# Kernel tuning notes

Measured on AMD Instinct MI355X. Metric: run time of the kernel, lower is better.

## Reference

```python
import jax, jax.numpy as jnp
import numpy as np

N = 100000   # num nodes
E = 20000    # num hyperedges
D = 128      # feature dim
NNZ = 600000 # incidences
EPS = 1e-5


def setup_inputs() -> dict:
    key = jax.random.key(0)
    ks = jax.random.split(key, 16)
    src = jax.random.randint(ks[0], (NNZ,), 0, N)   # node indices
    edg = jax.random.randint(ks[1], (NNZ,), 0, E)   # hyperedge indices
    edge_index = jnp.stack([src, edg]).astype(jnp.int64)
    node_attr = jax.random.normal(ks[2], (N, D), jnp.float32)
    edge_attr = jax.random.normal(ks[3], (E, D), jnp.float32)  # unused by forward
    inp = {"edge_index": edge_index, "node_attr": node_attr, "edge_attr": edge_attr}
    for l in range(3):
        inp[f"W{l+1}"] = jax.random.normal(ks[4 + l], (D, D), jnp.float32) / np.float32(np.sqrt(D))
        inp[f"b{l+1}"] = jnp.zeros((D,), jnp.float32)
        inp[f"g{l+1}"] = jnp.ones((D,), jnp.float32)
        inp[f"beta{l+1}"] = jnp.zeros((D,), jnp.float32)
    return inp


def _hconv(x, W, b, src, edg):
    # PyG HypergraphConv (no attention): out = D^{-1} H W_e B^{-1} H^T (X Theta) + b, W_e = I
    x = x @ W
    ones = jnp.ones(src.shape, x.dtype)
    deg_n = jax.ops.segment_sum(ones, src, num_segments=N)  # node degree
    deg_e = jax.ops.segment_sum(ones, edg, num_segments=E)  # hyperedge size
    Dinv = jnp.where(deg_n > 0, 1.0 / deg_n, 0.0)
    Binv = jnp.where(deg_e > 0, 1.0 / deg_e, 0.0)
    # node -> hyperedge: m_e = B^{-1} sum_{i in e} x_i
    e_feat = Binv[:, None] * jax.ops.segment_sum(x[src], edg, num_segments=E)
    # hyperedge -> node: out_i = D^{-1} sum_{e ni i} m_e
    out = Dinv[:, None] * jax.ops.segment_sum(e_feat[edg], src, num_segments=N)
    return out + b


def _bn(x, g, beta):
    # BatchNorm1d, training mode (biased variance over nodes)
    mu = jnp.mean(x, axis=0)
    var = jnp.mean((x - mu) ** 2, axis=0)
    return g * (x - mu) / jnp.sqrt(var + EPS) + beta


def reference(edge_index, node_attr, edge_attr,
              W1, b1, g1, beta1, W2, b2, g2, beta2, W3, b3, g3, beta3):
    src, edg = edge_index[0], edge_index[1]
    x = _bn(jax.nn.relu(_hconv(node_attr, W1, b1, src, edg)), g1, beta1)
    x = _bn(jax.nn.relu(_hconv(x, W2, b2, src, edg)), g2, beta2)
    x = _bn(jax.nn.relu(_hconv(x, W3, b3, src, edg)), g3, beta3)
    return x
```

## Files before the change

### kernel.cpp

```cpp
#include <hip/hip_runtime.h>
#include <stdint.h>

#define DIM 128

static inline int cdiv(long a, long b) { return (int)((a + b - 1) / b); }

typedef float f32x4 __attribute__((ext_vector_type(4)));

__device__ __forceinline__ unsigned pk_bf16(float a, float b) {
  unsigned ua = __float_as_uint(a), ub = __float_as_uint(b);
  ua = (ua + 0x7FFFu + ((ua >> 16) & 1u)) >> 16;
  ub = (ub + 0x7FFFu + ((ub >> 16) & 1u)) >> 16;
  return ua | (ub << 16);
}
__device__ __forceinline__ float bf_lo(unsigned u) { return __uint_as_float(u << 16); }
__device__ __forceinline__ float bf_hi(unsigned u) { return __uint_as_float(u & 0xFFFF0000u); }

__global__ __launch_bounds__(256) void count_kernel(
    const int* __restrict__ raw, int* __restrict__ src, int* __restrict__ edg,
    int* __restrict__ cnt, int E, int nnz) {
  bool is64;
  {
    int l = threadIdx.x & 63;
    int v = raw[2 * l + 1];
    unsigned long long m = __ballot(v == 0);
    is64 = (m == ~0ull);
  }
  int g = blockIdx.x * 256 + threadIdx.x;
  if (g < nnz) {
    int s = is64 ? raw[2 * g] : raw[g];
    int e = is64 ? raw[2 * (nnz + g)] : raw[nnz + g];
    src[g] = s;
    edg[g] = e;
    atomicAdd(&cnt[e], 1);
    atomicAdd(&cnt[E + s], 1);
  }
}

__global__ __launch_bounds__(256) void scanA_kernel(
    const int* __restrict__ cnt, int* __restrict__ P, int* __restrict__ BS, int M) {
  __shared__ int lds[256];
  int t = threadIdx.x;
  long base = blockIdx.x * 1024L;
  int v[4], ts = 0;
#pragma unroll
  for (int j = 0; j < 4; ++j) {
    long i = base + t * 4 + j;
    v[j] = (i < M) ? cnt[i] : 0;
    ts += v[j];
  }
  lds[t] = ts;
  __syncthreads();
  for (int off = 1; off < 256; off <<= 1) {
    int x = (t >= off) ? lds[t - off] : 0;
    __syncthreads();
    lds[t] += x;
    __syncthreads();
  }
  int run = lds[t] - ts;
#pragma unroll
  for (int j = 0; j < 4; ++j) {
    long i = base + t * 4 + j;
    if (i < M) P[i] = run;
    run += v[j];
  }
  if (t == 255) BS[blockIdx.x] = lds[255];
}

__global__ void scanB_kernel(int* __restrict__ BS, int* __restrict__ P,
                             int nblocks, int M) {
  if (threadIdx.x == 0) {
    int run = 0;
    for (int i = 0; i < nblocks; ++i) { int x = BS[i]; BS[i] = run; run += x; }
    P[M] = run;
  }
}

__global__ __launch_bounds__(256) void scanC_kernel(
    int* __restrict__ P, const int* __restrict__ BS, int M) {
  long i = blockIdx.x * 256L + threadIdx.x;
  if (i < M) P[i] += BS[i >> 10];
}

__global__ __launch_bounds__(256) void fill_adj_kernel(
    const int* __restrict__ src, const int* __restrict__ edg,
    const int* __restrict__ P, int* __restrict__ cnt,
    int* __restrict__ adj_e, int* __restrict__ adj_n, int E, int nnz) {
  int g = blockIdx.x * 256 + threadIdx.x;
  if (g < nnz) {
    int e = edg[g], s = src[g];
    int pe = P[e] + atomicAdd(&cnt[e], 1);
    adj_e[pe] = s;
    int pn = P[E + s] - nnz + atomicAdd(&cnt[E + s], 1);
    adj_n[pn] = e;
  }
}

__global__ void prep_w_kernel(const float* __restrict__ W,
                              const float* __restrict__ sums,
                              const float* __restrict__ sumsq,
                              const float* __restrict__ gprev,
                              const float* __restrict__ betaprev,
                              float* __restrict__ Wp, float* __restrict__ rvec,
                              int has_aff, float inv_n) {
  __shared__ float sa[DIM], sd[DIM];
  int j = threadIdx.x;
  if (has_aff) {
    float mu = sums[j] * inv_n;
    float var = fmaf(sumsq[j], inv_n, -mu * mu);
    float a = gprev[j] * rsqrtf(var + 1e-5f);
    sa[j] = a;
    sd[j] = fmaf(-mu, a, betaprev[j]);
  } else {
    sa[j] = 1.0f;
    sd[j] = 0.0f;
  }
  __syncthreads();
  float racc = 0.0f;
  for (int c = 0; c < DIM; ++c) {
    float w = W[c * DIM + j];
    Wp[c * DIM + j] = sa[c] * w;
    racc = fmaf(sd[c], w, racc);
  }
  rvec[j] = racc;
}

__global__ __launch_bounds__(256) void edge_gather_f32_kernel(
    const float4* __restrict__ X4, const int* __restrict__ P,
    const int* __restrict__ adj_e, float* __restrict__ ag, int E) {
  int slot = threadIdx.x >> 5;
  int l = threadIdx.x & 31;
  int e = blockIdx.x * 8 + slot;
  if (e >= E) return;
  int p0 = P[e], p1 = P[e + 1];
  float4 a = {0.f, 0.f, 0.f, 0.f};
  int kl = p1 - 1;
  for (int k = p0; k < p1; k += 8) {
    int n0 = adj_e[min(k, kl)];
    int n1 = adj_e[min(k + 1, kl)];
    int n2 = adj_e[min(k + 2, kl)];
    int n3 = adj_e[min(k + 3, kl)];
    int n4 = adj_e[min(k + 4, kl)];
    int n5 = adj_e[min(k + 5, kl)];
    int n6 = adj_e[min(k + 6, kl)];
    int n7 = adj_e[min(k + 7, kl)];
    float4 q0 = X4[(size_t)n0 * 32 + l];
    float4 q1 = X4[(size_t)n1 * 32 + l];
    float4 q2 = X4[(size_t)n2 * 32 + l];
    float4 q3 = X4[(size_t)n3 * 32 + l];
    float4 q4 = X4[(size_t)n4 * 32 + l];
    float4 q5 = X4[(size_t)n5 * 32 + l];
    float4 q6 = X4[(size_t)n6 * 32 + l];
    float4 q7 = X4[(size_t)n7 * 32 + l];
    a.x += ((q0.x + q1.x) + (q2.x + q3.x)) + ((q4.x + q5.x) + (q6.x + q7.x));
    a.y += ((q0.y + q1.y) + (q2.y + q3.y)) + ((q4.y + q5.y) + (q6.y + q7.y));
    a.z += ((q0.z + q1.z) + (q2.z + q3.z)) + ((q4.z + q5.z) + (q6.z + q7.z));
    a.w += ((q0.w + q1.w) + (q2.w + q3.w)) + ((q4.w + q5.w) + (q6.w + q7.w));
  }
  int deg = p1 - p0;
  if (deg > 0) {
    int extra = ((deg + 7) & ~7) - deg;
    if (extra) {
      float4 ql = X4[(size_t)adj_e[kl] * 32 + l];
      float ex = (float)extra;
      a.x -= ex * ql.x; a.y -= ex * ql.y; a.z -= ex * ql.z; a.w -= ex * ql.w;
    }
  }
  float binv = (deg > 0) ? 1.0f / (float)deg : 0.0f;
  f32x4 o;
  o.x = a.x * binv; o.y = a.y * binv; o.z = a.z * binv; o.w = a.w * binv;
  __builtin_nontemporal_store(o, &((f32x4*)ag)[(size_t)e * 32 + l]);
}

__global__ __launch_bounds__(256) void edge_gather_bf16_kernel(
    const uint2* __restrict__ xh, const int* __restrict__ P,
    const int* __restrict__ adj_e, float* __restrict__ ag, int E) {
  int slot = threadIdx.x >> 5;
  int l = threadIdx.x & 31;
  int e = blockIdx.x * 8 + slot;
  if (e >= E) return;
  int p0 = P[e], p1 = P[e + 1];
  float4 a = {0.f, 0.f, 0.f, 0.f};
  int kl = p1 - 1;
  for (int k = p0; k < p1; k += 8) {
    int n0 = adj_e[min(k, kl)];
    int n1 = adj_e[min(k + 1, kl)];
    int n2 = adj_e[min(k + 2, kl)];
    int n3 = adj_e[min(k + 3, kl)];
    int n4 = adj_e[min(k + 4, kl)];
    int n5 = adj_e[min(k + 5, kl)];
    int n6 = adj_e[min(k + 6, kl)];
    int n7 = adj_e[min(k + 7, kl)];
    uint2 q0 = xh[(size_t)n0 * 32 + l];
    uint2 q1 = xh[(size_t)n1 * 32 + l];
    uint2 q2 = xh[(size_t)n2 * 32 + l];
    uint2 q3 = xh[(size_t)n3 * 32 + l];
    uint2 q4 = xh[(size_t)n4 * 32 + l];
    uint2 q5 = xh[(size_t)n5 * 32 + l];
    uint2 q6 = xh[(size_t)n6 * 32 + l];
    uint2 q7 = xh[(size_t)n7 * 32 + l];
    a.x += ((bf_lo(q0.x) + bf_lo(q1.x)) + (bf_lo(q2.x) + bf_lo(q3.x))) +
           ((bf_lo(q4.x) + bf_lo(q5.x)) + (bf_lo(q6.x) + bf_lo(q7.x)));
    a.y += ((bf_hi(q0.x) + bf_hi(q1.x)) + (bf_hi(q2.x) + bf_hi(q3.x))) +
           ((bf_hi(q4.x) + bf_hi(q5.x)) + (bf_hi(q6.x) + bf_hi(q7.x)));
    a.z += ((bf_lo(q0.y) + bf_lo(q1.y)) + (bf_lo(q2.y) + bf_lo(q3.y))) +
           ((bf_lo(q4.y) + bf_lo(q5.y)) + (bf_lo(q6.y) + bf_lo(q7.y)));
    a.w += ((bf_hi(q0.y) + bf_hi(q1.y)) + (bf_hi(q2.y) + bf_hi(q3.y))) +
           ((bf_hi(q4.y) + bf_hi(q5.y)) + (bf_hi(q6.y) + bf_hi(q7.y)));
  }
  int deg = p1 - p0;
  if (deg > 0) {
    int extra = ((deg + 7) & ~7) - deg;
    if (extra) {
      uint2 ql = xh[(size_t)adj_e[kl] * 32 + l];
      float ex = (float)extra;
      a.x -= ex * bf_lo(ql.x); a.y -= ex * bf_hi(ql.x);
      a.z -= ex * bf_lo(ql.y); a.w -= ex * bf_hi(ql.y);
    }
  }
  float binv = (deg > 0) ? 1.0f / (float)deg : 0.0f;
  f32x4 o;
  o.x = a.x * binv; o.y = a.y * binv; o.z = a.z * binv; o.w = a.w * binv;
  __builtin_nontemporal_store(o, &((f32x4*)ag)[(size_t)e * 32 + l]);
}

__global__ __launch_bounds__(256) void gemm128_kernel(
    const float* __restrict__ X, const float* __restrict__ Wp,
    const float* __restrict__ rvec, const int* __restrict__ Pdeg,
    unsigned* __restrict__ Yh, int nrows) {
  __shared__ float sW[32 * DIM];
  __shared__ float sX[DIM * 36];
  const int t = threadIdx.x;
  const int row0 = blockIdx.x * DIM;
  const int tx = t & 15, ty = t >> 4;
  const int col0 = tx * 8, lr0 = ty * 8;
  float acc[8][8];
#pragma unroll
  for (int i = 0; i < 8; ++i)
#pragma unroll
    for (int j = 0; j < 8; ++j) acc[i][j] = 0.0f;

  for (int kc = 0; kc < 4; ++kc) {
    __syncthreads();
    {
      const float4* W4 = (const float4*)(Wp + kc * 32 * DIM);
      float4* sW4 = (float4*)sW;
#pragma unroll
      for (int i = 0; i < 4; ++i) sW4[t + i * 256] = W4[t + i * 256];
    }
#pragma unroll
    for (int i = 0; i < 4; ++i) {
      int q = t + i * 256;
      int rr = q >> 3, kq = q & 7;
      int gr = row0 + rr; if (gr >= nrows) gr = nrows - 1;
      float4 v = *(const float4*)&X[(size_t)gr * DIM + kc * 32 + kq * 4];
      *(float4*)&sX[rr * 36 + kq * 4] = v;
    }
    __syncthreads();
    for (int kk = 0; kk < 32; ++kk) {
      float4 w0 = *(const float4*)&sW[kk * DIM + col0];
      float4 w1 = *(const float4*)&sW[kk * DIM + col0 + 4];
      float wv[8] = {w0.x, w0.y, w0.z, w0.w, w1.x, w1.y, w1.z, w1.w};
      float xv[8];
#pragma unroll
      for (int i = 0; i < 8; ++i) xv[i] = sX[(lr0 + i) * 36 + kk];
#pragma unroll
      for (int i = 0; i < 8; ++i)
#pragma unroll
        for (int j = 0; j < 8; ++j) acc[i][j] = fmaf(xv[i], wv[j], acc[i][j]);
    }
  }
  float4 r0 = *(const float4*)&rvec[col0];
  float4 r1 = *(const float4*)&rvec[col0 + 4];
#pragma unroll
  for (int i = 0; i < 8; ++i) {
    int gr = row0 + lr0 + i;
    if (gr < nrows) {
      float nz = (Pdeg[gr + 1] > Pdeg[gr]) ? 1.0f : 0.0f;
      float o0x = (acc[i][0] + r0.x) * nz, o0y = (acc[i][1] + r0.y) * nz;
      float o0z = (acc[i][2] + r0.z) * nz, o0w = (acc[i][3] + r0.w) * nz;
      float o1x = (acc[i][4] + r1.x) * nz, o1y = (acc[i][5] + r1.y) * nz;
      float o1z = (acc[i][6] + r1.z) * nz, o1w = (acc[i][7] + r1.w) * nz;
      uint4 st;
      st.x = pk_bf16(o0x, o0y);
      st.y = pk_bf16(o0z, o0w);
      st.z = pk_bf16(o1x, o1y);
      st.w = pk_bf16(o1z, o1w);
      *(uint4*)&Yh[(size_t)gr * 64 + (col0 >> 1)] = st;
    }
  }
}

__global__ __launch_bounds__(256) void node_gather_kernel(
    const uint2* __restrict__ ef, const int* __restrict__ P,
    const int* __restrict__ adj_n, const float* __restrict__ b,
    uint2* __restrict__ zh, float* __restrict__ sum,
    float* __restrict__ sumsq, int E, int N, int nnz) {
  __shared__ float lsum[DIM], lsumsq[DIM];
  int t = threadIdx.x;
  if (t < DIM) { lsum[t] = 0.f; lsumsq[t] = 0.f; }
  __syncthreads();
  int slot = t >> 5;
  int l = t & 31;
  float4 bc = ((const float4*)b)[l];
  float4 s1 = {0.f, 0.f, 0.f, 0.f}, s2 = {0.f, 0.f, 0.f, 0.f};
  for (int i = blockIdx.x * 8 + slot; i < N; i += gridDim.x * 8) {
    int p0 = P[E + i] - nnz, p1 = P[E + i + 1] - nnz;
    float4 a = {0.f, 0.f, 0.f, 0.f};
    int kl = p1 - 1;
    for (int k = p0; k < p1; k += 8) {
      int e0 = adj_n[min(k, kl)];
      int e1 = adj_n[min(k + 1, kl)];
      int e2 = adj_n[min(k + 2, kl)];
      int e3 = adj_n[min(k + 3, kl)];
      int e4 = adj_n[min(k + 4, kl)];
      int e5 = adj_n[min(k + 5, kl)];
      int e6 = adj_n[min(k + 6, kl)];
      int e7 = adj_n[min(k + 7, kl)];
      uint2 q0 = ef[(size_t)e0 * 32 + l];
      uint2 q1 = ef[(size_t)e1 * 32 + l];
      uint2 q2 = ef[(size_t)e2 * 32 + l];
      uint2 q3 = ef[(size_t)e3 * 32 + l];
      uint2 q4 = ef[(size_t)e4 * 32 + l];
      uint2 q5 = ef[(size_t)e5 * 32 + l];
      uint2 q6 = ef[(size_t)e6 * 32 + l];
      uint2 q7 = ef[(size_t)e7 * 32 + l];
      a.x += ((bf_lo(q0.x) + bf_lo(q1.x)) + (bf_lo(q2.x) + bf_lo(q3.x))) +
             ((bf_lo(q4.x) + bf_lo(q5.x)) + (bf_lo(q6.x) + bf_lo(q7.x)));
      a.y += ((bf_hi(q0.x) + bf_hi(q1.x)) + (bf_hi(q2.x) + bf_hi(q3.x))) +
             ((bf_hi(q4.x) + bf_hi(q5.x)) + (bf_hi(q6.x) + bf_hi(q7.x)));
      a.z += ((bf_lo(q0.y) + bf_lo(q1.y)) + (bf_lo(q2.y) + bf_lo(q3.y))) +
             ((bf_lo(q4.y) + bf_lo(q5.y)) + (bf_lo(q6.y) + bf_lo(q7.y)));
      a.w += ((bf_hi(q0.y) + bf_hi(q1.y)) + (bf_hi(q2.y) + bf_hi(q3.y))) +
             ((bf_hi(q4.y) + bf_hi(q5.y)) + (bf_hi(q6.y) + bf_hi(q7.y)));
    }
    int deg = p1 - p0;
    if (deg > 0) {
      int extra = ((deg + 7) & ~7) - deg;
      if (extra) {
        uint2 ql = ef[(size_t)adj_n[kl] * 32 + l];
        float ex = (float)extra;
        a.x -= ex * bf_lo(ql.x); a.y -= ex * bf_hi(ql.x);
        a.z -= ex * bf_lo(ql.y); a.w -= ex * bf_hi(ql.y);
      }
    }
    float dinv = (deg > 0) ? 1.0f / (float)deg : 0.0f;
    float4 v;
    v.x = fmaxf(fmaf(dinv, a.x, bc.x), 0.f);
    v.y = fmaxf(fmaf(dinv, a.y, bc.y), 0.f);
    v.z = fmaxf(fmaf(dinv, a.z, bc.z), 0.f);
    v.w = fmaxf(fmaf(dinv, a.w, bc.w), 0.f);
    uint2 o;
    o.x = pk_bf16(v.x, v.y);
    o.y = pk_bf16(v.z, v.w);
    zh[(size_t)i * 32 + l] = o;
    s1.x += v.x; s1.y += v.y; s1.z += v.z; s1.w += v.w;
    s2.x = fmaf(v.x, v.x, s2.x); s2.y = fmaf(v.y, v.y, s2.y);
    s2.z = fmaf(v.z, v.z, s2.z); s2.w = fmaf(v.w, v.w, s2.w);
  }
  int c0 = l * 4;
  atomicAdd(&lsum[c0 + 0], s1.x); atomicAdd(&lsum[c0 + 1], s1.y);
  atomicAdd(&lsum[c0 + 2], s1.z); atomicAdd(&lsum[c0 + 3], s1.w);
  atomicAdd(&lsumsq[c0 + 0], s2.x); atomicAdd(&lsumsq[c0 + 1], s2.y);
  atomicAdd(&lsumsq[c0 + 2], s2.z); atomicAdd(&lsumsq[c0 + 3], s2.w);
  __syncthreads();
  if (t < DIM) {
    atomicAdd(&sum[t], lsum[t]);
    atomicAdd(&sumsq[t], lsumsq[t]);
  }
}

__global__ void finalize_bn_kernel(const float* __restrict__ sum,
                                   const float* __restrict__ sumsq,
                                   const float* __restrict__ g,
                                   const float* __restrict__ beta,
                                   float* __restrict__ aff_a, float* __restrict__ aff_d,
                                   int n) {
  int c = threadIdx.x;
  float inv_n = 1.0f / (float)n;
  float mu = sum[c] * inv_n;
  float var = fmaf(sumsq[c], inv_n, -mu * mu);
  float a = g[c] * rsqrtf(var + 1e-5f);
  aff_a[c] = a;
  aff_d[c] = fmaf(-mu, a, beta[c]);
}

__global__ __launch_bounds__(256) void apply_affine_kernel(
    const uint2* __restrict__ zh, const float* __restrict__ aff_a,
    const float* __restrict__ aff_d, float* __restrict__ out, long total4) {
  long i = blockIdx.x * 256L + threadIdx.x;
  if (i >= total4) return;
  int c4 = (int)(i & 31);
  float4 a = ((const float4*)aff_a)[c4];
  float4 d = ((const float4*)aff_d)[c4];
  uint2 q = zh[i];
  f32x4 o;
  o.x = fmaf(a.x, bf_lo(q.x), d.x);
  o.y = fmaf(a.y, bf_hi(q.x), d.y);
  o.z = fmaf(a.z, bf_lo(q.y), d.z);
  o.w = fmaf(a.w, bf_hi(q.y), d.w);
  __builtin_nontemporal_store(o, &((f32x4*)out)[i]);
}

extern "C" void kernel_launch(void* const* d_in, const int* in_sizes, int n_in,
                              void* d_out, int out_size, void* d_ws, size_t ws_size,
                              hipStream_t stream) {
  const int NNZv = in_sizes[0] / 2;
  const int Nv   = in_sizes[1] / DIM;
  const int Ev   = in_sizes[2] / DIM;
  const int* eidx_raw = (const int*)d_in[0];
  const float* node_attr = (const float*)d_in[1];

  float* bufE  = (float*)d_ws;
  float* Wp    = bufE + (size_t)Ev * DIM;
  float* rvec  = Wp + DIM * DIM;
  float* sums  = rvec + 128;
  float* sumsq = sums + 128;
  float* aff_a = sumsq + 128;
  float* aff_d = aff_a + 128;
  int* src   = (int*)(aff_d + 128);
  int* edg   = src + NNZv;
  int* cnt   = edg + NNZv;
  int* P     = cnt + (((size_t)Ev + Nv + 3) & ~(size_t)3);
  int* BS    = P + (((size_t)Ev + Nv + 1 + 3) & ~(size_t)3);
  int* adj_e = BS + 256;
  int* adj_n = adj_e + NNZv;
  unsigned* efh = (unsigned*)src;
  uint2* xh = (uint2*)(adj_n + NNZv);

  const int M = Ev + Nv;
  const int nbA = cdiv(M, 1024);
  const float inv_n = 1.0f / (float)Nv;

  hipMemsetAsync(cnt, 0, (size_t)M * 4, stream);
  count_kernel<<<cdiv(NNZv, 256), 256, 0, stream>>>(eidx_raw, src, edg, cnt, Ev, NNZv);
  scanA_kernel<<<nbA, 256, 0, stream>>>(cnt, P, BS, M);
  scanB_kernel<<<1, 64, 0, stream>>>(BS, P, nbA, M);
  scanC_kernel<<<cdiv(M, 256), 256, 0, stream>>>(P, BS, M);
  hipMemsetAsync(cnt, 0, (size_t)M * 4, stream);
  fill_adj_kernel<<<cdiv(NNZv, 256), 256, 0, stream>>>(src, edg, P, cnt, adj_e, adj_n, Ev, NNZv);

  for (int l = 0; l < 3; ++l) {
    const float* W     = (const float*)d_in[3 + l * 4];
    const float* b     = (const float*)d_in[4 + l * 4];
    const float* gprev    = (const float*)d_in[5 + (l > 0 ? l - 1 : 0) * 4];
    const float* betaprev = (const float*)d_in[6 + (l > 0 ? l - 1 : 0) * 4];

    prep_w_kernel<<<1, 128, 0, stream>>>(W, sums, sumsq, gprev, betaprev,
                                         Wp, rvec, l > 0 ? 1 : 0, inv_n);
    if (l == 0)
      edge_gather_f32_kernel<<<cdiv(Ev, 8), 256, 0, stream>>>(
          (const float4*)node_attr, P, adj_e, bufE, Ev);
    else
      edge_gather_bf16_kernel<<<cdiv(Ev, 8), 256, 0, stream>>>(
          xh, P, adj_e, bufE, Ev);
    gemm128_kernel<<<cdiv(Ev, DIM), 256, 0, stream>>>(bufE, Wp, rvec, P, efh, Ev);
    hipMemsetAsync(sums, 0, 256 * 4, stream);
    node_gather_kernel<<<2048, 256, 0, stream>>>(
        (const uint2*)efh, P, adj_n, b, xh, sums, sumsq, Ev, Nv, NNZv);
  }
  {
    const float* g2    = (const float*)d_in[5 + 2 * 4];
    const float* beta2 = (const float*)d_in[6 + 2 * 4];
    finalize_bn_kernel<<<1, 128, 0, stream>>>(sums, sumsq, g2, beta2, aff_a, aff_d, Nv);
  }
  apply_affine_kernel<<<cdiv((long)Nv * 32, 256), 256, 0, stream>>>(
      xh, aff_a, aff_d, (float*)d_out, (long)Nv * 32);
}
```

Before: 714.4 us.

## Use zero sentinel rows for gather padding and fold small launches into neighbours

```diff
diff --git a/kernel.cpp b/kernel.cpp
--- a/kernel.cpp
+++ b/kernel.cpp
@@ -15,6 +15,17 @@
 }
 __device__ __forceinline__ float bf_lo(unsigned u) { return __uint_as_float(u << 16); }
 __device__ __forceinline__ float bf_hi(unsigned u) { return __uint_as_float(u & 0xFFFF0000u); }
+
+__device__ __forceinline__ void acc8(float4& a, const uint2* q) {
+  a.x += ((bf_lo(q[0].x) + bf_lo(q[1].x)) + (bf_lo(q[2].x) + bf_lo(q[3].x))) +
+         ((bf_lo(q[4].x) + bf_lo(q[5].x)) + (bf_lo(q[6].x) + bf_lo(q[7].x)));
+  a.y += ((bf_hi(q[0].x) + bf_hi(q[1].x)) + (bf_hi(q[2].x) + bf_hi(q[3].x))) +
+         ((bf_hi(q[4].x) + bf_hi(q[5].x)) + (bf_hi(q[6].x) + bf_hi(q[7].x)));
+  a.z += ((bf_lo(q[0].y) + bf_lo(q[1].y)) + (bf_lo(q[2].y) + bf_lo(q[3].y))) +
+         ((bf_lo(q[4].y) + bf_lo(q[5].y)) + (bf_lo(q[6].y) + bf_lo(q[7].y)));
+  a.w += ((bf_hi(q[0].y) + bf_hi(q[1].y)) + (bf_hi(q[2].y) + bf_hi(q[3].y))) +
+         ((bf_hi(q[4].y) + bf_hi(q[5].y)) + (bf_hi(q[6].y) + bf_hi(q[7].y)));
+}
 
 __global__ __launch_bounds__(256) void count_kernel(
     const int* __restrict__ raw, int* __restrict__ src, int* __restrict__ edg,
@@ -77,9 +88,12 @@
 }
 
 __global__ __launch_bounds__(256) void scanC_kernel(
-    int* __restrict__ P, const int* __restrict__ BS, int M) {
+    int* __restrict__ P, const int* __restrict__ BS, int* __restrict__ cnt, int M) {
   long i = blockIdx.x * 256L + threadIdx.x;
-  if (i < M) P[i] += BS[i >> 10];
+  if (i < M) {
+    P[i] += BS[i >> 10];
+    cnt[i] = 0;
+  }
 }
 
 __global__ __launch_bounds__(256) void fill_adj_kernel(
@@ -96,33 +110,41 @@
   }
 }
 
-__global__ void prep_w_kernel(const float* __restrict__ W,
-                              const float* __restrict__ sums,
-                              const float* __restrict__ sumsq,
-                              const float* __restrict__ gprev,
-                              const float* __restrict__ betaprev,
-                              float* __restrict__ Wp, float* __restrict__ rvec,
-                              int has_aff, float inv_n) {
+__global__ __launch_bounds__(1024) void prep_w_kernel(
+    const float* __restrict__ W, float* __restrict__ sums,
+    float* __restrict__ sumsq, const float* __restrict__ gprev,
+    const float* __restrict__ betaprev, float* __restrict__ Wp,
+    float* __restrict__ rvec, int has_aff, float inv_n) {
   __shared__ float sa[DIM], sd[DIM];
-  int j = threadIdx.x;
-  if (has_aff) {
-    float mu = sums[j] * inv_n;
-    float var = fmaf(sumsq[j], inv_n, -mu * mu);
-    float a = gprev[j] * rsqrtf(var + 1e-5f);
-    sa[j] = a;
-    sd[j] = fmaf(-mu, a, betaprev[j]);
-  } else {
-    sa[j] = 1.0f;
-    sd[j] = 0.0f;
-  }
-  __syncthreads();
-  float racc = 0.0f;
-  for (int c = 0; c < DIM; ++c) {
+  __shared__ float red[1024];
+  int t = threadIdx.x;
+  if (t < DIM) {
+    float a = 1.0f, d = 0.0f;
+    if (has_aff) {
+      float mu = sums[t] * inv_n;
+      float var = fmaf(sumsq[t], inv_n, -mu * mu);
+      a = gprev[t] * rsqrtf(var + 1e-5f);
+      d = fmaf(-mu, a, betaprev[t]);
+    }
+    sa[t] = a; sd[t] = d;
+  }
+  __syncthreads();
+  if (t < DIM) { sums[t] = 0.f; sumsq[t] = 0.f; }
+  int j = t & 127, grp = t >> 7;
+  float racc = 0.f;
+  for (int c = grp; c < DIM; c += 8) {
     float w = W[c * DIM + j];
     Wp[c * DIM + j] = sa[c] * w;
     racc = fmaf(sd[c], w, racc);
   }
-  rvec[j] = racc;
+  red[t] = racc;
+  __syncthreads();
+  if (t < DIM) {
+    float r = 0.f;
+#pragma unroll
+    for (int g2 = 0; g2 < 8; ++g2) r += red[j + g2 * 128];
+    rvec[j] = r;
+  }
 }
 
 __global__ __launch_bounds__(256) void edge_gather_f32_kernel(
@@ -174,7 +196,7 @@
 
 __global__ __launch_bounds__(256) void edge_gather_bf16_kernel(
     const uint2* __restrict__ xh, const int* __restrict__ P,
-    const int* __restrict__ adj_e, float* __restrict__ ag, int E) {
+    const int* __restrict__ adj_e, float* __restrict__ ag, int E, int SENT) {
   int slot = threadIdx.x >> 5;
   int l = threadIdx.x & 31;
   int e = blockIdx.x * 8 + slot;
@@ -182,42 +204,18 @@
   int p0 = P[e], p1 = P[e + 1];
   float4 a = {0.f, 0.f, 0.f, 0.f};
   int kl = p1 - 1;
-  for (int k = p0; k < p1; k += 8) {
-    int n0 = adj_e[min(k, kl)];
-    int n1 = adj_e[min(k + 1, kl)];
-    int n2 = adj_e[min(k + 2, kl)];
-    int n3 = adj_e[min(k + 3, kl)];
-    int n4 = adj_e[min(k + 4, kl)];
-    int n5 = adj_e[min(k + 5, kl)];
-    int n6 = adj_e[min(k + 6, kl)];
-    int n7 = adj_e[min(k + 7, kl)];
-    uint2 q0 = xh[(size_t)n0 * 32 + l];
-    uint2 q1 = xh[(size_t)n1 * 32 + l];
-    uint2 q2 = xh[(size_t)n2 * 32 + l];
-    uint2 q3 = xh[(size_t)n3 * 32 + l];
-    uint2 q4 = xh[(size_t)n4 * 32 + l];
-    uint2 q5 = xh[(size_t)n5 * 32 + l];
-    uint2 q6 = xh[(size_t)n6 * 32 + l];
-    uint2 q7 = xh[(size_t)n7 * 32 + l];
-    a.x += ((bf_lo(q0.x) + bf_lo(q1.x)) + (bf_lo(q2.x) + bf_lo(q3.x))) +
-           ((bf_lo(q4.x) + bf_lo(q5.x)) + (bf_lo(q6.x) + bf_lo(q7.x)));
-    a.y += ((bf_hi(q0.x) + bf_hi(q1.x)) + (bf_hi(q2.x) + bf_hi(q3.x))) +
-           ((bf_hi(q4.x) + bf_hi(q5.x)) + (bf_hi(q6.x) + bf_hi(q7.x)));
-    a.z += ((bf_lo(q0.y) + bf_lo(q1.y)) + (bf_lo(q2.y) + bf_lo(q3.y))) +
-           ((bf_lo(q4.y) + bf_lo(q5.y)) + (bf_lo(q6.y) + bf_lo(q7.y)));
-    a.w += ((bf_hi(q0.y) + bf_hi(q1.y)) + (bf_hi(q2.y) + bf_hi(q3.y))) +
-           ((bf_hi(q4.y) + bf_hi(q5.y)) + (bf_hi(q6.y) + bf_hi(q7.y)));
+  for (int k = p0; k < p1; k += 16) {
+    int n[16];
+    n[0] = adj_e[k];
+#pragma unroll
+    for (int j = 1; j < 16; ++j) n[j] = (k + j <= kl) ? adj_e[k + j] : SENT;
+    uint2 q[16];
+#pragma unroll
+    for (int j = 0; j < 16; ++j) q[j] = xh[(size_t)n[j] * 32 + l];
+    acc8(a, q);
+    acc8(a, q + 8);
   }
   int deg = p1 - p0;
-  if (deg > 0) {
-    int extra = ((deg + 7) & ~7) - deg;
-    if (extra) {
-      uint2 ql = xh[(size_t)adj_e[kl] * 32 + l];
-      float ex = (float)extra;
-      a.x -= ex * bf_lo(ql.x); a.y -= ex * bf_hi(ql.x);
-      a.z -= ex * bf_lo(ql.y); a.w -= ex * bf_hi(ql.y);
-    }
-  }
   float binv = (deg > 0) ? 1.0f / (float)deg : 0.0f;
   f32x4 o;
   o.x = a.x * binv; o.y = a.y * binv; o.z = a.z * binv; o.w = a.w * binv;
@@ -295,7 +293,7 @@
     const uint2* __restrict__ ef, const int* __restrict__ P,
     const int* __restrict__ adj_n, const float* __restrict__ b,
     uint2* __restrict__ zh, float* __restrict__ sum,
-    float* __restrict__ sumsq, int E, int N, int nnz) {
+    float* __restrict__ sumsq, int E, int N, int nnz, int SENT) {
   __shared__ float lsum[DIM], lsumsq[DIM];
   int t = threadIdx.x;
   if (t < DIM) { lsum[t] = 0.f; lsumsq[t] = 0.f; }
@@ -309,41 +307,26 @@
     float4 a = {0.f, 0.f, 0.f, 0.f};
     int kl = p1 - 1;
     for (int k = p0; k < p1; k += 8) {
-      int e0 = adj_n[min(k, kl)];
-      int e1 = adj_n[min(k + 1, kl)];
-      int e2 = adj_n[min(k + 2, kl)];
-      int e3 = adj_n[min(k + 3, kl)];
-      int e4 = adj_n[min(k + 4, kl)];
-      int e5 = adj_n[min(k + 5, kl)];
-      int e6 = adj_n[min(k + 6, kl)];
-      int e7 = adj_n[min(k + 7, kl)];
-      uint2 q0 = ef[(size_t)e0 * 32 + l];
-      uint2 q1 = ef[(size_t)e1 * 32 + l];
-      uint2 q2 = ef[(size_t)e2 * 32 + l];
-      uint2 q3 = ef[(size_t)e3 * 32 + l];
-      uint2 q4 = ef[(size_t)e4 * 32 + l];
-      uint2 q5 = ef[(size_t)e5 * 32 + l];
-      uint2 q6 = ef[(size_t)e6 * 32 + l];
-      uint2 q7 = ef[(size_t)e7 * 32 + l];
-      a.x += ((bf_lo(q0.x) + bf_lo(q1.x)) + (bf_lo(q2.x) + bf_lo(q3.x))) +
-             ((bf_lo(q4.x) + bf_lo(q5.x)) + (bf_lo(q6.x) + bf_lo(q7.x)));
-      a.y += ((bf_hi(q0.x) + bf_hi(q1.x)) + (bf_hi(q2.x) + bf_hi(q3.x))) +
-             ((bf_hi(q4.x) + bf_hi(q5.x)) + (bf_hi(q6.x) + bf_hi(q7.x)));
-      a.z += ((bf_lo(q0.y) + bf_lo(q1.y)) + (bf_lo(q2.y) + bf_lo(q3.y))) +
-             ((bf_lo(q4.y) + bf_lo(q5.y)) + (bf_lo(q6.y) + bf_lo(q7.y)));
-      a.w += ((bf_hi(q0.y) + bf_hi(q1.y)) + (bf_hi(q2.y) + bf_hi(q3.y))) +
-             ((bf_hi(q4.y) + bf_hi(q5.y)) + (bf_hi(q6.y) + bf_hi(q7.y)));
+      int e0 = adj_n[k];
+      int e1 = (k + 1 <= kl) ? adj_n[k + 1] : SENT;
+      int e2 = (k + 2 <= kl) ? adj_n[k + 2] : SENT;
+      int e3 = (k + 3 <= kl) ? adj_n[k + 3] : SENT;
+      int e4 = (k + 4 <= kl) ? adj_n[k + 4] : SENT;
+      int e5 = (k + 5 <= kl) ? adj_n[k + 5] : SENT;
+      int e6 = (k + 6 <= kl) ? adj_n[k + 6] : SENT;
+      int e7 = (k + 7 <= kl) ? adj_n[k + 7] : SENT;
+      uint2 q[8];
+      q[0] = ef[(size_t)e0 * 32 + l];
+      q[1] = ef[(size_t)e1 * 32 + l];
+      q[2] = ef[(size_t)e2 * 32 + l];
+      q[3] = ef[(size_t)e3 * 32 + l];
+      q[4] = ef[(size_t)e4 * 32 + l];
+      q[5] = ef[(size_t)e5 * 32 + l];
+      q[6] = ef[(size_t)e6 * 32 + l];
+      q[7] = ef[(size_t)e7 * 32 + l];
+      acc8(a, q);
     }
     int deg = p1 - p0;
-    if (deg > 0) {
-      int extra = ((deg + 7) & ~7) - deg;
-      if (extra) {
-        uint2 ql = ef[(size_t)adj_n[kl] * 32 + l];
-        float ex = (float)extra;
-        a.x -= ex * bf_lo(ql.x); a.y -= ex * bf_hi(ql.x);
-        a.z -= ex * bf_lo(ql.y); a.w -= ex * bf_hi(ql.y);
-      }
-    }
     float dinv = (deg > 0) ? 1.0f / (float)deg : 0.0f;
     float4 v;
     v.x = fmaxf(fmaf(dinv, a.x, bc.x), 0.f);
@@ -370,35 +353,30 @@
   }
 }
 
-__global__ void finalize_bn_kernel(const float* __restrict__ sum,
-                                   const float* __restrict__ sumsq,
-                                   const float* __restrict__ g,
-                                   const float* __restrict__ beta,
-                                   float* __restrict__ aff_a, float* __restrict__ aff_d,
-                                   int n) {
-  int c = threadIdx.x;
-  float inv_n = 1.0f / (float)n;
-  float mu = sum[c] * inv_n;
-  float var = fmaf(sumsq[c], inv_n, -mu * mu);
-  float a = g[c] * rsqrtf(var + 1e-5f);
-  aff_a[c] = a;
-  aff_d[c] = fmaf(-mu, a, beta[c]);
-}
-
 __global__ __launch_bounds__(256) void apply_affine_kernel(
-    const uint2* __restrict__ zh, const float* __restrict__ aff_a,
-    const float* __restrict__ aff_d, float* __restrict__ out, long total4) {
-  long i = blockIdx.x * 256L + threadIdx.x;
+    const uint2* __restrict__ zh, const float* __restrict__ sums,
+    const float* __restrict__ sumsq, const float* __restrict__ g,
+    const float* __restrict__ beta, float* __restrict__ out,
+    long total4, float inv_n) {
+  __shared__ float sa[DIM], sd[DIM];
+  int t = threadIdx.x;
+  if (t < DIM) {
+    float mu = sums[t] * inv_n;
+    float var = fmaf(sumsq[t], inv_n, -mu * mu);
+    float a = g[t] * rsqrtf(var + 1e-5f);
+    sa[t] = a;
+    sd[t] = fmaf(-mu, a, beta[t]);
+  }
+  __syncthreads();
+  long i = blockIdx.x * 256L + t;
   if (i >= total4) return;
-  int c4 = (int)(i & 31);
-  float4 a = ((const float4*)aff_a)[c4];
-  float4 d = ((const float4*)aff_d)[c4];
+  int c0 = (int)(i & 31) * 4;
   uint2 q = zh[i];
   f32x4 o;
-  o.x = fmaf(a.x, bf_lo(q.x), d.x);
-  o.y = fmaf(a.y, bf_hi(q.x), d.y);
-  o.z = fmaf(a.z, bf_lo(q.y), d.z);
-  o.w = fmaf(a.w, bf_hi(q.y), d.w);
+  o.x = fmaf(sa[c0 + 0], bf_lo(q.x), sd[c0 + 0]);
+  o.y = fmaf(sa[c0 + 1], bf_hi(q.x), sd[c0 + 1]);
+  o.z = fmaf(sa[c0 + 2], bf_lo(q.y), sd[c0 + 2]);
+  o.w = fmaf(sa[c0 + 3], bf_hi(q.y), sd[c0 + 3]);
   __builtin_nontemporal_store(o, &((f32x4*)out)[i]);
 }
 
@@ -436,9 +414,10 @@
   count_kernel<<<cdiv(NNZv, 256), 256, 0, stream>>>(eidx_raw, src, edg, cnt, Ev, NNZv);
   scanA_kernel<<<nbA, 256, 0, stream>>>(cnt, P, BS, M);
   scanB_kernel<<<1, 64, 0, stream>>>(BS, P, nbA, M);
-  scanC_kernel<<<cdiv(M, 256), 256, 0, stream>>>(P, BS, M);
-  hipMemsetAsync(cnt, 0, (size_t)M * 4, stream);
+  scanC_kernel<<<cdiv(M, 256), 256, 0, stream>>>(P, BS, cnt, M);
   fill_adj_kernel<<<cdiv(NNZv, 256), 256, 0, stream>>>(src, edg, P, cnt, adj_e, adj_n, Ev, NNZv);
+  hipMemsetAsync(efh + (size_t)Ev * 64, 0, 256, stream);
+  hipMemsetAsync(xh + (size_t)Nv * 32, 0, 256, stream);
 
   for (int l = 0; l < 3; ++l) {
     const float* W     = (const float*)d_in[3 + l * 4];
@@ -446,24 +425,22 @@
     const float* gprev    = (const float*)d_in[5 + (l > 0 ? l - 1 : 0) * 4];
     const float* betaprev = (const float*)d_in[6 + (l > 0 ? l - 1 : 0) * 4];
 
-    prep_w_kernel<<<1, 128, 0, stream>>>(W, sums, sumsq, gprev, betaprev,
-                                         Wp, rvec, l > 0 ? 1 : 0, inv_n);
+    prep_w_kernel<<<1, 1024, 0, stream>>>(W, sums, sumsq, gprev, betaprev,
+                                          Wp, rvec, l > 0 ? 1 : 0, inv_n);
     if (l == 0)
       edge_gather_f32_kernel<<<cdiv(Ev, 8), 256, 0, stream>>>(
           (const float4*)node_attr, P, adj_e, bufE, Ev);
     else
       edge_gather_bf16_kernel<<<cdiv(Ev, 8), 256, 0, stream>>>(
-          xh, P, adj_e, bufE, Ev);
+          xh, P, adj_e, bufE, Ev, Nv);
     gemm128_kernel<<<cdiv(Ev, DIM), 256, 0, stream>>>(bufE, Wp, rvec, P, efh, Ev);
-    hipMemsetAsync(sums, 0, 256 * 4, stream);
     node_gather_kernel<<<2048, 256, 0, stream>>>(
-        (const uint2*)efh, P, adj_n, b, xh, sums, sumsq, Ev, Nv, NNZv);
+        (const uint2*)efh, P, adj_n, b, xh, sums, sumsq, Ev, Nv, NNZv, Ev);
   }
   {
     const float* g2    = (const float*)d_in[5 + 2 * 4];
     const float* beta2 = (const float*)d_in[6 + 2 * 4];
-    finalize_bn_kernel<<<1, 128, 0, stream>>>(sums, sumsq, g2, beta2, aff_a, aff_d, Nv);
-  }
-  apply_affine_kernel<<<cdiv((long)Nv * 32, 256), 256, 0, stream>>>(
-      xh, aff_a, aff_d, (float*)d_out, (long)Nv * 32);
-}
+    apply_affine_kernel<<<cdiv((long)Nv * 32, 256), 256, 0, stream>>>(
+        xh, sums, sumsq, g2, beta2, (float*)d_out, (long)Nv * 32, inv_n);
+  }
+}
```

Result: faster. 671.8 us (-6.0%).
